# Optimization experiments

Hardware: AMD Instinct MI355X
Metric: run time of the kernel (lower is better)

Reference implementation:

```python
import jax, jax.numpy as jnp
import numpy as np

M = 4  # mixture size of the AttentionStem value embedding

def unfold_windows(a, kh, kw, Hout, Wout):
    # a: [..., Hp, Wp] -> [..., Hout, Wout, kh, kw] (stride-1 sliding windows, cropped)
    rows = []
    for i in range(kh):
        cols = [a[..., i:i + Hout, j:j + Wout] for j in range(kw)]
        rows.append(jnp.stack(cols, axis=-1))
    return jnp.stack(rows, axis=-2)

def attention_stem(x, qw, kw_, vw, emb_a, emb_b, emb_mix, kh, kw, pad):
    # x: [B,Cin,H,W]; qw/kw_: [Cin,Co]; vw: [M,Cin,Co]; emb_a:[Co,kh]; emb_b:[Co,kw]; emb_mix:[M,Co]
    B, Cin, H, W = x.shape
    pl, pr, pt, pb = pad  # F.pad order (left,right,top,bottom)
    xp = jnp.pad(x, ((0, 0), (0, 0), (pt, pb), (pl, pr)))
    Hp, Wp = xp.shape[2], xp.shape[3]
    Hout = min(Hp - kh + 1, H)
    Wout = min(Wp - kw + 1, W)
    q = jnp.einsum('bchw,co->bohw', x[:, :, :Hout, :Wout], qw)       # 1x1 conv query
    k = jnp.einsum('bchw,co->bohw', xp, kw_)                          # 1x1 conv key on padded
    v = jnp.einsum('bchw,mco->mbohw', xp, vw)                         # m 1x1 conv values
    k_win = unfold_windows(k, kh, kw, Hout, Wout)                     # [B,Co,Ho,Wo,kh,kw]
    v_win = unfold_windows(v, kh, kw, Hout, Wout)                     # [M,B,Co,Ho,Wo,kh,kw]
    # mixture relative-position embedding, softmax over mixtures per (kh,kw) offset
    la = emb_mix @ emb_a                                              # [M,kh]
    lb = emb_mix @ emb_b                                              # [M,kw]
    emb = jax.nn.softmax(la[:, :, None] + lb[:, None, :], axis=0)     # [M,kh,kw]
    v_agg = jnp.einsum('mkl,mbohwkl->bohwkl', emb, v_win)             # [B,Co,Ho,Wo,kh,kw]
    K = kh * kw
    scores = jnp.einsum('bohw,bohwkl->bhwkl', q, k_win).reshape(B, Hout, Wout, K)
    attn = jax.nn.softmax(scores, axis=-1).reshape(B, Hout, Wout, kh, kw)
    out = jnp.einsum('bhwkl,bohwkl->bohw', attn, v_agg)               # [B,Co,Ho,Wo]
    return out

def bn_relu(x, g, b):
    # training-mode BatchNorm2d + ReLU
    mu = x.mean(axis=(0, 2, 3), keepdims=True)
    var = x.var(axis=(0, 2, 3), keepdims=True)
    y = (x - mu) * jax.lax.rsqrt(var + 1e-5) * g[None, :, None, None] + b[None, :, None, None]
    return jax.nn.relu(y)

def _params(key):
    ks = jax.random.split(key, 18)
    def w(k, shape):
        return jax.random.normal(k, shape, dtype=jnp.float32) * 0.1
    cfg = [(1, 64, 1, 5), (64, 128, 2, 5), (128, 16, 2, 5)]
    p = {}
    i = 0
    for s, (ci, co, kh, kw) in enumerate(cfg):
        p[f'p{s}_q'] = w(ks[i], (ci, co)); i += 1
        p[f'p{s}_k'] = w(ks[i], (ci, co)); i += 1
        p[f'p{s}_v'] = w(ks[i], (M, ci, co)); i += 1
        p[f'p{s}_ea'] = w(ks[i], (co, kh)); i += 1
        p[f'p{s}_eb'] = w(ks[i], (co, kw)); i += 1
        p[f'p{s}_em'] = w(ks[i], (M, co)); i += 1
        p[f'p{s}_g'] = jnp.ones((co,), jnp.float32)
        p[f'p{s}_b'] = jnp.zeros((co,), jnp.float32)
    return p

def setup_inputs() -> dict:
    key = jax.random.key(0)
    kx, kp = jax.random.split(key)
    inp = {'x': jax.random.normal(kx, (2, 1, 8, 3000), dtype=jnp.float32)}
    inp.update(_params(kp))
    return inp

def reference(x,
              p0_q, p0_k, p0_v, p0_ea, p0_eb, p0_em, p0_g, p0_b,
              p1_q, p1_k, p1_v, p1_ea, p1_eb, p1_em, p1_g, p1_b,
              p2_q, p2_k, p2_v, p2_ea, p2_eb, p2_em, p2_g, p2_b):
    h = attention_stem(x, p0_q, p0_k, p0_v, p0_ea, p0_eb, p0_em, 1, 5, (2, 2, 0, 0))
    h = bn_relu(h, p0_g, p0_b)[:, :, ::2, ::2]                        # MaxPool2d(1,2) == stride-2 subsample
    h = attention_stem(h, p1_q, p1_k, p1_v, p1_ea, p1_eb, p1_em, 2, 5, (2, 2, 1, 1))
    h = bn_relu(h, p1_g, p1_b)[:, :, ::2, ::2]
    h = attention_stem(h, p2_q, p2_k, p2_v, p2_ea, p2_eb, p2_em, 2, 5, (2, 2, 0, 0))
    h = bn_relu(h, p2_g, p2_b)
    B, C, H, W = h.shape
    nW = W // 56                                                       # AvgPool2d((1,56))
    return h[:, :, :, :nW * 56].reshape(B, C, H, nW, 56).mean(-1)
```

## Files before the change

kernel.cpp:

```cpp
#include <hip/hip_runtime.h>
#include <math.h>


#define TPB 256

__global__ void prep0_kernel(const float* __restrict__ ea,
                             const float* __restrict__ eb,
                             const float* __restrict__ em,
                             const float* __restrict__ qw,
                             const float* __restrict__ kw_,
                             const float* __restrict__ vw,
                             float* __restrict__ par) {
    const int M4 = 4, Co = 64, kw = 5;
    __shared__ float la[4];
    __shared__ float lb[20];
    __shared__ float embs[20];
    int tid = threadIdx.x;
    if (tid < 64) {
        float p = qw[tid] * kw_[tid];
#pragma unroll
        for (int d = 1; d < 64; d <<= 1) p += __shfl_xor(p, d, 64);
        if (tid == 0) par[0] = p;
    }
    if (tid >= 64 && tid < 64 + M4) {
        int m = tid - 64;
        float s = 0.f;
        for (int o = 0; o < Co; ++o) s += em[m * Co + o] * ea[o];
        la[m] = s;
    }
    if (tid >= 128 && tid < 128 + M4 * kw) {
        int r = tid - 128;
        int m = r / kw, l = r % kw;
        float s = 0.f;
        for (int o = 0; o < Co; ++o) s += em[m * Co + o] * eb[o * kw + l];
        lb[m * kw + l] = s;
    }
    __syncthreads();
    if (tid < 5) {
        float lg[4];
        float mx = -1e30f;
        for (int m = 0; m < M4; ++m) {
            lg[m] = la[m] + lb[m * kw + tid];
            mx = fmaxf(mx, lg[m]);
        }
        float sum = 0.f;
        for (int m = 0; m < M4; ++m) { lg[m] = expf(lg[m] - mx); sum += lg[m]; }
        float inv = 1.f / sum;
        for (int m = 0; m < M4; ++m) embs[tid * 4 + m] = lg[m] * inv;
    }
    __syncthreads();
    for (int e = tid; e < 5 * 64; e += blockDim.x) {
        int t = e / 64, o = e - t * 64;
        float s = 0.f;
        for (int m = 0; m < M4; ++m) s += embs[t * 4 + m] * vw[m * 64 + o];
        par[1 + e] = s;
    }
}

__global__ void prep_wcat_kernel(const float* __restrict__ ea,
                                 const float* __restrict__ eb,
                                 const float* __restrict__ em,
                                 const float* __restrict__ qw,
                                 const float* __restrict__ kw_,
                                 const float* __restrict__ vw,
                                 float* __restrict__ Wcat,
                                 int Co, int kh, int kw, int Cin,
                                 const float2* __restrict__ part,
                                 float* __restrict__ mr,
                                 int Cprev, int NCH, int count) {
    const int M4 = 4;
    __shared__ float la[8];
    __shared__ float lb[20];
    __shared__ float embs[40];
    int K = kh * kw;
    int tid = threadIdx.x;
    if (blockIdx.x == 0 && tid < Cprev) {
        double s = 0.0, s2 = 0.0;
        for (int i = 0; i < NCH; ++i) {
            float2 p = part[(size_t)tid * NCH + i];
            s += p.x; s2 += p.y;
        }
        double mean = s / count;
        double var = s2 / count - mean * mean;
        mr[tid] = (float)mean;
        mr[Cprev + tid] = (float)(1.0 / sqrt(var + 1e-5));
    }
    if (tid < M4 * kh) {
        int m = tid / kh, k = tid % kh;
        float s = 0.f;
        for (int o = 0; o < Co; ++o) s += em[m * Co + o] * ea[o * kh + k];
        la[tid] = s;
    }
    if (tid >= 64 && tid < 64 + M4 * kw) {
        int r = tid - 64;
        int m = r / kw, l = r % kw;
        float s = 0.f;
        for (int o = 0; o < Co; ++o) s += em[m * Co + o] * eb[o * kw + l];
        lb[r] = s;
    }
    __syncthreads();
    if (tid < K) {
        int k = tid / kw, l = tid % kw;
        float lg[4];
        float mx = -1e30f;
        for (int m = 0; m < M4; ++m) {
            lg[m] = la[m * kh + k] + lb[m * kw + l];
            mx = fmaxf(mx, lg[m]);
        }
        float sum = 0.f;
        for (int m = 0; m < M4; ++m) { lg[m] = expf(lg[m] - mx); sum += lg[m]; }
        float inv = 1.f / sum;
        for (int m = 0; m < M4; ++m) embs[tid * 4 + m] = lg[m] * inv;
    }
    __syncthreads();
    int Mtot = (2 + K) * Co;
    long long total = (long long)Mtot * Cin;
    for (long long e = (long long)blockIdx.x * blockDim.x + tid; e < total;
         e += (long long)gridDim.x * blockDim.x) {
        int m = (int)(e / Cin);
        int c = (int)(e - (long long)m * Cin);
        float val;
        if (m < Co) {
            val = qw[c * Co + m];
        } else if (m < 2 * Co) {
            val = kw_[c * Co + (m - Co)];
        } else {
            int mz = m - 2 * Co;
            int t = mz / Co;
            int o = mz - t * Co;
            val = 0.f;
            for (int mm = 0; mm < M4; ++mm)
                val += embs[t * 4 + mm] * vw[(mm * Cin + c) * Co + o];
        }
        Wcat[e] = val;
    }
}

__global__ void attn_out0_kernel(const float* __restrict__ x,
                                 const float* __restrict__ par,
                                 float* __restrict__ s0,
                                 float2* __restrict__ part0) {
    __shared__ float wsh[5][256];
    __shared__ float vsh[5 * 64];
    int tid = threadIdx.x;
    int b = blockIdx.y;
    int n0 = blockIdx.x * 256;
    int n = n0 + tid;
    for (int i = tid; i < 320; i += 256) vsh[i] = par[1 + i];
    float c0 = par[0];
    if (n < 24000) {
        int h = n / 3000, w = n - h * 3000;
        const float* xr = x + b * 24000 + h * 3000;
        float xc = xr[w];
        float xs[5], s[5];
#pragma unroll
        for (int t = 0; t < 5; ++t) {
            int col = w + t - 2;
            xs[t] = (col >= 0 && col < 3000) ? xr[col] : 0.f;
            s[t] = c0 * xc * xs[t];
        }
        float mx = s[0];
#pragma unroll
        for (int t = 1; t < 5; ++t) mx = fmaxf(mx, s[t]);
        float sum = 0.f;
#pragma unroll
        for (int t = 0; t < 5; ++t) { s[t] = expf(s[t] - mx); sum += s[t]; }
        float inv = 1.f / sum;
#pragma unroll
        for (int t = 0; t < 5; ++t) wsh[t][tid] = s[t] * inv * xs[t];
    } else {
#pragma unroll
        for (int t = 0; t < 5; ++t) wsh[t][tid] = 0.f;
    }
    __syncthreads();
    int jq = tid & 63, og = tid >> 6;
    int nq = n0 + jq * 4;
    bool st = (nq < 24000);
    float wq[5][4];
#pragma unroll
    for (int t = 0; t < 5; ++t)
#pragma unroll
        for (int j = 0; j < 4; ++j) wq[t][j] = wsh[t][jq * 4 + j];
    int obase = og * 16;
    int chunk = b * gridDim.x + blockIdx.x;
    for (int oi = 0; oi < 16; ++oi) {
        int o = obase + oi;
        float4 v = make_float4(0.f, 0.f, 0.f, 0.f);
#pragma unroll
        for (int t = 0; t < 5; ++t) {
            float vo = vsh[t * 64 + o];
            v.x = fmaf(wq[t][0], vo, v.x);
            v.y = fmaf(wq[t][1], vo, v.y);
            v.z = fmaf(wq[t][2], vo, v.z);
            v.w = fmaf(wq[t][3], vo, v.w);
        }
        if (st) *(float4*)&s0[((size_t)b * 64 + o) * 24000 + nq] = v;
        float ls = v.x + v.y + v.z + v.w;
        float ls2 = v.x * v.x + v.y * v.y + v.z * v.z + v.w * v.w;
#pragma unroll
        for (int d = 1; d < 64; d <<= 1) {
            ls += __shfl_xor(ls, d, 64);
            ls2 += __shfl_xor(ls2, d, 64);
        }
        if ((tid & 63) == 0)
            part0[(size_t)o * 188 + chunk] = make_float2(ls, ls2);
    }
}

__launch_bounds__(256, 4)
__global__ void gemm_qkz_kernel(const float* __restrict__ A,
                                const float* __restrict__ X,
                                float* __restrict__ qk,
                                float* __restrict__ z,
                                int M, int N, int K, int twoCo) {
    __shared__ float As[32][132];
    __shared__ float Bs[32][132];
    int tid = threadIdx.x;
    int b = blockIdx.z;
    int m0 = blockIdx.y * 128, n0 = blockIdx.x * 128;
    int Mz = M - twoCo;
    float acc[8][8] = {{0.f}};
    int am = tid >> 1, ak = (tid & 1) * 16;
    int bk = tid >> 3, bn = (tid & 7) * 16;
    int tm = tid & 15, tn = tid >> 4;

    for (int k0 = 0; k0 < K; k0 += 32) {
        {
            int mA = m0 + am;
            const float* Ap = A + (size_t)mA * K + k0 + ak;
#pragma unroll
            for (int q = 0; q < 4; ++q) {
                float4 v = (mA < M) ? *(const float4*)(Ap + q * 4)
                                    : make_float4(0.f, 0.f, 0.f, 0.f);
                int kk = ak + q * 4;
                As[kk + 0][am] = v.x;
                As[kk + 1][am] = v.y;
                As[kk + 2][am] = v.z;
                As[kk + 3][am] = v.w;
            }
        }
        {
            const float* Xp = X + (size_t)b * K * N + (size_t)(k0 + bk) * N + n0 + bn;
            if (n0 + 128 <= N) {
#pragma unroll
                for (int q = 0; q < 4; ++q)
                    *(float4*)&Bs[bk][bn + q * 4] = *(const float4*)(Xp + q * 4);
            } else {
#pragma unroll
                for (int q = 0; q < 16; ++q) {
                    int n = n0 + bn + q;
                    Bs[bk][bn + q] = (n < N) ? Xp[q] : 0.f;
                }
            }
        }
        __syncthreads();
#pragma unroll 8
        for (int k = 0; k < 32; ++k) {
            float4 a0 = *(const float4*)&As[k][tm * 4];
            float4 a1 = *(const float4*)&As[k][64 + tm * 4];
            float4 b0 = *(const float4*)&Bs[k][tn * 4];
            float4 b1 = *(const float4*)&Bs[k][64 + tn * 4];
            float av[8] = {a0.x, a0.y, a0.z, a0.w, a1.x, a1.y, a1.z, a1.w};
            float bv[8] = {b0.x, b0.y, b0.z, b0.w, b1.x, b1.y, b1.z, b1.w};
#pragma unroll
            for (int i = 0; i < 8; ++i)
#pragma unroll
                for (int j = 0; j < 8; ++j)
                    acc[i][j] = fmaf(av[i], bv[j], acc[i][j]);
        }
        __syncthreads();
    }
    bool fullN = (n0 + 128 <= N);
#pragma unroll
    for (int iq = 0; iq < 2; ++iq) {
        int mb = m0 + iq * 64 + tm * 4;
        if (mb >= M) continue;
        if (mb < twoCo) {
#pragma unroll
            for (int jq = 0; jq < 2; ++jq)
#pragma unroll
                for (int jj = 0; jj < 4; ++jj) {
                    int n = n0 + jq * 64 + tn * 4 + jj;
                    if (n < N) {
                        float4 v = make_float4(acc[iq * 4 + 0][jq * 4 + jj],
                                               acc[iq * 4 + 1][jq * 4 + jj],
                                               acc[iq * 4 + 2][jq * 4 + jj],
                                               acc[iq * 4 + 3][jq * 4 + jj]);
                        *(float4*)&qk[((size_t)b * N + n) * twoCo + mb] = v;
                    }
                }
        } else {
#pragma unroll
            for (int i = 0; i < 4; ++i) {
                int row = mb + i - twoCo;
                float* zp = &z[((size_t)b * Mz + row) * N];
#pragma unroll
                for (int jq = 0; jq < 2; ++jq) {
                    int nb_ = n0 + jq * 64 + tn * 4;
                    if (fullN) {
                        *(float4*)&zp[nb_] = make_float4(acc[iq * 4 + i][jq * 4 + 0],
                                                         acc[iq * 4 + i][jq * 4 + 1],
                                                         acc[iq * 4 + i][jq * 4 + 2],
                                                         acc[iq * 4 + i][jq * 4 + 3]);
                    } else {
#pragma unroll
                        for (int jj = 0; jj < 4; ++jj)
                            if (nb_ + jj < N) zp[nb_ + jj] = acc[iq * 4 + i][jq * 4 + jj];
                    }
                }
            }
        }
    }
}

template <int KH, int KW, int CO, int NPB>
__global__ void attn_v3_kernel(const float* __restrict__ qk,
                               float* __restrict__ attn,
                               int H, int W, int Ho, int Wo, int pt, int pl) {
    const int K = KH * KW;
    __shared__ float ssh[NPB][K];
    int tid = threadIdx.x;
    int b = blockIdx.y;
    int ln = tid / K, t = tid - ln * K;
    int Nout = Ho * Wo;
    int n = blockIdx.x * NPB + ln;
    bool active = (tid < NPB * K) && (n < Nout);
    int HWin = H * W;
    float sv = 0.f;
    if (active) {
        int ho = n / Wo, wo = n - ho * Wo;
        int row = ho + t / KW - pt, col = wo + t % KW - pl;
        if (row >= 0 && row < H && col >= 0 && col < W) {
            const float* qp = qk + ((size_t)b * HWin + ho * W + wo) * (2 * CO);
            const float* kp = qk + ((size_t)b * HWin + (size_t)row * W + col) * (2 * CO) + CO;
#pragma unroll
            for (int o = 0; o < CO; o += 4) {
                float4 q4 = *(const float4*)(qp + o);
                float4 k4 = *(const float4*)(kp + o);
                sv += q4.x * k4.x + q4.y * k4.y + q4.z * k4.z + q4.w * k4.w;
            }
        }
        ssh[ln][t] = sv;
    }
    __syncthreads();
    if (active) {
        float mx = ssh[ln][0];
#pragma unroll
        for (int tt = 1; tt < K; ++tt) mx = fmaxf(mx, ssh[ln][tt]);
        float sum = 0.f;
#pragma unroll
        for (int tt = 0; tt < K; ++tt) sum += expf(ssh[ln][tt] - mx);
        float num = expf(sv - mx);
        attn[((size_t)b * K + t) * Nout + n] = num / sum;
    }
}

template <int KH, int KW>
__global__ void combine_stats_kernel(const float* __restrict__ z,
                                     const float* __restrict__ attn,
                                     float* __restrict__ out,
                                     float2* __restrict__ part,
                                     int Co, int Mz,
                                     int H, int W, int Ho, int Wo,
                                     int pt, int pl) {
    const int K = KH * KW;
    int tid = threadIdx.x;
    int bc = blockIdx.y;
    int b = bc / Co, o = bc - b * Co;
    int Nout = Ho * Wo, Nin = H * W;
    int n = blockIdx.x * blockDim.x + tid;
    float val = 0.f;
    if (n < Nout) {
        int ho = n / Wo, wo = n - ho * Wo;
#pragma unroll
        for (int dk = 0; dk < KH; ++dk) {
            int row = ho + dk - pt;
            if (row < 0 || row >= H) continue;
#pragma unroll
            for (int dl = 0; dl < KW; ++dl) {
                int col = wo + dl - pl;
                if (col < 0 || col >= W) continue;
                int t = dk * KW + dl;
                float a = attn[((size_t)b * K + t) * Nout + n];
                float zv = z[((size_t)b * Mz + t * Co + o) * Nin + row * W + col];
                val = fmaf(a, zv, val);
            }
        }
        out[((size_t)b * Co + o) * Nout + n] = val;
    }
    __shared__ float sh[TPB], sh2[TPB];
    sh[tid] = (n < Nout) ? val : 0.f;
    sh2[tid] = (n < Nout) ? val * val : 0.f;
    __syncthreads();
    for (int st = TPB / 2; st > 0; st >>= 1) {
        if (tid < st) { sh[tid] += sh[tid + st]; sh2[tid] += sh2[tid + st]; }
        __syncthreads();
    }
    if (tid == 0) {
        int chunk = b * gridDim.x + blockIdx.x;
        part[(size_t)o * (2 * gridDim.x) + chunk] = make_float2(sh[0], sh2[0]);
    }
}

__global__ void bn_pool_kernel(const float* __restrict__ x,
                               const float* __restrict__ mr,
                               const float* __restrict__ g,
                               const float* __restrict__ bb,
                               float* __restrict__ y,
                               int B, int C, int H, int W, int H2, int W2) {
    int idx = blockIdx.x * blockDim.x + threadIdx.x;
    int N = B * C * H2 * W2;
    if (idx >= N) return;
    int w2 = idx % W2; int r = idx / W2;
    int h2 = r % H2; r /= H2;
    int c = r % C; int b = r / C;
    float v = x[(((long long)b * C + c) * H + 2 * h2) * W + 2 * w2];
    float yn = (v - mr[c]) * mr[C + c] * g[c] + bb[c];
    y[idx] = fmaxf(yn, 0.f);
}

__global__ void bn_avg_final_kernel(const float* __restrict__ x,
                                    const float2* __restrict__ part,
                                    const float* __restrict__ g,
                                    const float* __restrict__ bb,
                                    float* __restrict__ out,
                                    int B, int C, int W, int nW, int NCH) {
    int idx = blockIdx.x * blockDim.x + threadIdx.x;
    int N = B * C * nW;
    if (idx >= N) return;
    int j = idx % nW; int r = idx / nW;
    int c = r % C; int b = r / C;
    double s = 0.0, s2 = 0.0;
    for (int i = 0; i < NCH; ++i) {
        float2 p = part[(size_t)c * NCH + i];
        s += p.x; s2 += p.y;
    }
    double cnt = (double)B * W;
    double mean = s / cnt;
    double var = s2 / cnt - mean * mean;
    float rstd = (float)(1.0 / sqrt(var + 1e-5));
    float meanf = (float)mean, gg = g[c], bo = bb[c];
    const float* xb = x + ((long long)b * C + c) * W + j * 56;
    float acc = 0.f;
    for (int i = 0; i < 56; ++i) {
        float yn = (xb[i] - meanf) * rstd * gg + bo;
        acc += fmaxf(yn, 0.f);
    }
    out[idx] = acc * (1.f / 56.f);
}

extern "C" void kernel_launch(void* const* d_in, const int* in_sizes, int n_in,
                              void* d_out, int out_size, void* d_ws, size_t ws_size,
                              hipStream_t stream) {
    const float* x   = (const float*)d_in[0];
    const float* qw0 = (const float*)d_in[1];
    const float* kw0 = (const float*)d_in[2];
    const float* vw0 = (const float*)d_in[3];
    const float* ea0 = (const float*)d_in[4];
    const float* eb0 = (const float*)d_in[5];
    const float* em0 = (const float*)d_in[6];
    const float* g0  = (const float*)d_in[7];
    const float* b0  = (const float*)d_in[8];
    const float* qw1 = (const float*)d_in[9];
    const float* kw1 = (const float*)d_in[10];
    const float* vw1 = (const float*)d_in[11];
    const float* ea1 = (const float*)d_in[12];
    const float* eb1 = (const float*)d_in[13];
    const float* em1 = (const float*)d_in[14];
    const float* g1  = (const float*)d_in[15];
    const float* b1  = (const float*)d_in[16];
    const float* qw2 = (const float*)d_in[17];
    const float* kw2 = (const float*)d_in[18];
    const float* vw2 = (const float*)d_in[19];
    const float* ea2 = (const float*)d_in[20];
    const float* eb2 = (const float*)d_in[21];
    const float* em2 = (const float*)d_in[22];
    const float* g2  = (const float*)d_in[23];
    const float* b2  = (const float*)d_in[24];
    float* outp = (float*)d_out;
    (void)ws_size; (void)in_sizes; (void)n_in; (void)out_size;

    float* ws = (float*)d_ws;
    size_t off = 0;
    auto alloc = [&](size_t n) { float* p = ws + off; off += (n + 63) & ~(size_t)63; return p; };

    float* arena = alloc(2 * 1280 * 6000);
    float* s0    = arena;
    float* z1    = arena;

    float* par0   = alloc(321);
    float* part0  = alloc(64 * 188 * 2);
    float* part1  = alloc(128 * 48 * 2);
    float* part2  = alloc(16 * 6 * 2);
    float* mr0    = alloc(2 * 64);
    float* h0     = alloc(2 * 64 * 6000);
    float* Wcat1  = alloc(1536 * 64);
    float* qk1    = alloc(2 * 6000 * 256);
    float* attn1  = alloc(2 * 10 * 6000);
    float* s1     = alloc(2 * 128 * 6000);
    float* mr1    = alloc(2 * 128);
    float* h1     = alloc(2 * 128 * 1500);
    float* Wcat2  = alloc(192 * 128);
    float* qk2    = alloc(2 * 1500 * 32);
    float* z2     = alloc(2 * 160 * 1500);
    float* attn2  = alloc(2 * 10 * 750);
    float* s2     = alloc(2 * 16 * 750);

    auto grid = [](int n) { return (n + TPB - 1) / TPB; };

    prep0_kernel<<<1, TPB, 0, stream>>>(ea0, eb0, em0, qw0, kw0, vw0, par0);
    {
        dim3 g(94, 2);
        attn_out0_kernel<<<g, TPB, 0, stream>>>(x, par0, s0, (float2*)part0);
    }
    prep_wcat_kernel<<<96, TPB, 0, stream>>>(ea1, eb1, em1, qw1, kw1, vw1, Wcat1,
        128, 2, 5, 64, (const float2*)part0, mr0, 64, 188, 48000);
    bn_pool_kernel<<<grid(2 * 64 * 6000), TPB, 0, stream>>>(s0, mr0, g0, b0, h0,
        2, 64, 8, 3000, 4, 1500);

    {
        dim3 g((6000 + 127) / 128, 1536 / 128, 2);
        gemm_qkz_kernel<<<g, TPB, 0, stream>>>(Wcat1, h0, qk1, z1, 1536, 6000, 64, 256);
    }
    {
        dim3 g(6000 / 25, 2);
        attn_v3_kernel<2, 5, 128, 25><<<g, TPB, 0, stream>>>(qk1, attn1,
            4, 1500, 4, 1500, 1, 2);
    }
    {
        dim3 g(24, 2 * 128);
        combine_stats_kernel<2, 5><<<g, TPB, 0, stream>>>(z1, attn1, s1,
            (float2*)part1, 128, 1280, 4, 1500, 4, 1500, 1, 2);
    }
    prep_wcat_kernel<<<24, TPB, 0, stream>>>(ea2, eb2, em2, qw2, kw2, vw2, Wcat2,
        16, 2, 5, 128, (const float2*)part1, mr1, 128, 48, 12000);
    bn_pool_kernel<<<grid(2 * 128 * 1500), TPB, 0, stream>>>(s1, mr1, g1, b1, h1,
        2, 128, 4, 1500, 2, 750);

    {
        dim3 g((1500 + 127) / 128, (192 + 127) / 128, 2);
        gemm_qkz_kernel<<<g, TPB, 0, stream>>>(Wcat2, h1, qk2, z2, 192, 1500, 128, 32);
    }
    {
        dim3 g(750 / 25, 2);
        attn_v3_kernel<2, 5, 16, 25><<<g, TPB, 0, stream>>>(qk2, attn2,
            2, 750, 1, 750, 0, 2);
    }
    {
        dim3 g(3, 2 * 16);
        combine_stats_kernel<2, 5><<<g, TPB, 0, stream>>>(z2, attn2, s2,
            (float2*)part2, 16, 160, 2, 750, 1, 750, 0, 2);
    }
    bn_avg_final_kernel<<<grid(2 * 16 * 13), TPB, 0, stream>>>(s2, (const float2*)part2,
        g2, b2, outp, 2, 16, 750, 13, 6);
}
```

Baseline: 282.2 us.

## Fuse BN+ReLU into GEMMs and replace stage-1 value path with attention-weighted GEMM

Stage 0 now writes only the stride-2 subsampled raw output instead of the full activation. BatchNorm+ReLU is applied on the fly inside the q/k GEMM and a new value GEMM, which drops the separate bn_pool passes. The value GEMM folds the attention weights into its B operand, so the large z1 tensor (1280 channels) is never materialised. It also writes only the subsampled output and emits per-block BN statistics. The cost is irregular gathers in the vgemm B-tile loads and small 64x64 tiles.

```diff
diff --git a/kernel.cpp b/kernel.cpp
--- a/kernel.cpp
+++ b/kernel.cpp
@@ -54,6 +54,154 @@
         float s = 0.f;
         for (int m = 0; m < M4; ++m) s += embs[t * 4 + m] * vw[m * 64 + o];
         par[1 + e] = s;
+    }
+}
+
+__global__ void attn_out0_kernel(const float* __restrict__ x,
+                                 const float* __restrict__ par,
+                                 float* __restrict__ h0raw,
+                                 float2* __restrict__ part0) {
+    __shared__ float wsh[5][256];
+    __shared__ float vsh[5 * 64];
+    int tid = threadIdx.x;
+    int b = blockIdx.y;
+    int n0 = blockIdx.x * 256;
+    int n = n0 + tid;
+    for (int i = tid; i < 320; i += 256) vsh[i] = par[1 + i];
+    float c0 = par[0];
+    if (n < 24000) {
+        int h = n / 3000, w = n - h * 3000;
+        const float* xr = x + b * 24000 + h * 3000;
+        float xc = xr[w];
+        float xs[5], s[5];
+#pragma unroll
+        for (int t = 0; t < 5; ++t) {
+            int col = w + t - 2;
+            xs[t] = (col >= 0 && col < 3000) ? xr[col] : 0.f;
+            s[t] = c0 * xc * xs[t];
+        }
+        float mx = s[0];
+#pragma unroll
+        for (int t = 1; t < 5; ++t) mx = fmaxf(mx, s[t]);
+        float sum = 0.f;
+#pragma unroll
+        for (int t = 0; t < 5; ++t) { s[t] = expf(s[t] - mx); sum += s[t]; }
+        float inv = 1.f / sum;
+#pragma unroll
+        for (int t = 0; t < 5; ++t) wsh[t][tid] = s[t] * inv * xs[t];
+    } else {
+#pragma unroll
+        for (int t = 0; t < 5; ++t) wsh[t][tid] = 0.f;
+    }
+    __syncthreads();
+    int jq = tid & 63, og = tid >> 6;
+    int nq = n0 + jq * 4;
+    int h = nq / 3000, w0 = nq - h * 3000;
+    bool st = (nq < 24000) && ((h & 1) == 0);
+    float wq[5][4];
+#pragma unroll
+    for (int t = 0; t < 5; ++t)
+#pragma unroll
+        for (int j = 0; j < 4; ++j) wq[t][j] = wsh[t][jq * 4 + j];
+    int obase = og * 16;
+    int chunk = b * gridDim.x + blockIdx.x;
+    for (int oi = 0; oi < 16; ++oi) {
+        int o = obase + oi;
+        float4 v = make_float4(0.f, 0.f, 0.f, 0.f);
+#pragma unroll
+        for (int t = 0; t < 5; ++t) {
+            float vo = vsh[t * 64 + o];
+            v.x = fmaf(wq[t][0], vo, v.x);
+            v.y = fmaf(wq[t][1], vo, v.y);
+            v.z = fmaf(wq[t][2], vo, v.z);
+            v.w = fmaf(wq[t][3], vo, v.w);
+        }
+        if (st) {
+            size_t base = ((size_t)b * 64 + o) * 6000 + (h >> 1) * 1500 + (w0 >> 1);
+            *(float2*)&h0raw[base] = make_float2(v.x, v.z);
+        }
+        float ls = v.x + v.y + v.z + v.w;
+        float ls2 = v.x * v.x + v.y * v.y + v.z * v.z + v.w * v.w;
+#pragma unroll
+        for (int d = 1; d < 64; d <<= 1) {
+            ls += __shfl_xor(ls, d, 64);
+            ls2 += __shfl_xor(ls2, d, 64);
+        }
+        if ((tid & 63) == 0)
+            part0[(size_t)o * 188 + chunk] = make_float2(ls, ls2);
+    }
+}
+
+__global__ void prep_stage1_kernel(const float* __restrict__ ea,
+                                   const float* __restrict__ eb,
+                                   const float* __restrict__ em,
+                                   const float* __restrict__ qw,
+                                   const float* __restrict__ kw_,
+                                   const float* __restrict__ vw,
+                                   float* __restrict__ Wqk,
+                                   float* __restrict__ Av,
+                                   const float2* __restrict__ part0,
+                                   float* __restrict__ mr0) {
+    const int M4 = 4, Co = 128, kh = 2, kw = 5, Cin = 64;
+    __shared__ float la[8];
+    __shared__ float lb[20];
+    __shared__ float embs[40];
+    int tid = threadIdx.x;
+    if (blockIdx.x == 0 && tid < 64) {
+        double s = 0.0, s2 = 0.0;
+        for (int i = 0; i < 188; ++i) {
+            float2 p = part0[(size_t)tid * 188 + i];
+            s += p.x; s2 += p.y;
+        }
+        double mean = s / 48000.0;
+        double var = s2 / 48000.0 - mean * mean;
+        mr0[tid] = (float)mean;
+        mr0[64 + tid] = (float)(1.0 / sqrt(var + 1e-5));
+    }
+    if (tid < M4 * kh) {
+        int m = tid / kh, k = tid % kh;
+        float s = 0.f;
+        for (int o = 0; o < Co; ++o) s += em[m * Co + o] * ea[o * kh + k];
+        la[tid] = s;
+    }
+    if (tid >= 64 && tid < 64 + M4 * kw) {
+        int r = tid - 64;
+        int m = r / kw, l = r % kw;
+        float s = 0.f;
+        for (int o = 0; o < Co; ++o) s += em[m * Co + o] * eb[o * kw + l];
+        lb[r] = s;
+    }
+    __syncthreads();
+    if (tid < 10) {
+        int k = tid / kw, l = tid % kw;
+        float lg[4];
+        float mx = -1e30f;
+        for (int m = 0; m < M4; ++m) {
+            lg[m] = la[m * kh + k] + lb[m * kw + l];
+            mx = fmaxf(mx, lg[m]);
+        }
+        float sum = 0.f;
+        for (int m = 0; m < M4; ++m) { lg[m] = expf(lg[m] - mx); sum += lg[m]; }
+        float inv = 1.f / sum;
+        for (int m = 0; m < M4; ++m) embs[tid * 4 + m] = lg[m] * inv;
+    }
+    __syncthreads();
+    const int TOT1 = 256 * 64;
+    const int TOT2 = 640 * 128;
+    for (int e = blockIdx.x * blockDim.x + tid; e < TOT1 + TOT2;
+         e += gridDim.x * blockDim.x) {
+        if (e < TOT1) {
+            int m = e / Cin, c = e - m * Cin;
+            Wqk[e] = (m < Co) ? qw[c * Co + m] : kw_[c * Co + (m - Co)];
+        } else {
+            int e2 = e - TOT1;
+            int k = e2 / Co, o = e2 - k * Co;
+            int c = k / 10, t = k - c * 10;
+            float val = 0.f;
+            for (int m = 0; m < M4; ++m)
+                val += embs[t * 4 + m] * vw[(m * Cin + c) * Co + o];
+            Av[e2] = val;
+        }
     }
 }
 
@@ -136,85 +284,18 @@
     }
 }
 
-__global__ void attn_out0_kernel(const float* __restrict__ x,
-                                 const float* __restrict__ par,
-                                 float* __restrict__ s0,
-                                 float2* __restrict__ part0) {
-    __shared__ float wsh[5][256];
-    __shared__ float vsh[5 * 64];
-    int tid = threadIdx.x;
-    int b = blockIdx.y;
-    int n0 = blockIdx.x * 256;
-    int n = n0 + tid;
-    for (int i = tid; i < 320; i += 256) vsh[i] = par[1 + i];
-    float c0 = par[0];
-    if (n < 24000) {
-        int h = n / 3000, w = n - h * 3000;
-        const float* xr = x + b * 24000 + h * 3000;
-        float xc = xr[w];
-        float xs[5], s[5];
-#pragma unroll
-        for (int t = 0; t < 5; ++t) {
-            int col = w + t - 2;
-            xs[t] = (col >= 0 && col < 3000) ? xr[col] : 0.f;
-            s[t] = c0 * xc * xs[t];
-        }
-        float mx = s[0];
-#pragma unroll
-        for (int t = 1; t < 5; ++t) mx = fmaxf(mx, s[t]);
-        float sum = 0.f;
-#pragma unroll
-        for (int t = 0; t < 5; ++t) { s[t] = expf(s[t] - mx); sum += s[t]; }
-        float inv = 1.f / sum;
-#pragma unroll
-        for (int t = 0; t < 5; ++t) wsh[t][tid] = s[t] * inv * xs[t];
-    } else {
-#pragma unroll
-        for (int t = 0; t < 5; ++t) wsh[t][tid] = 0.f;
-    }
-    __syncthreads();
-    int jq = tid & 63, og = tid >> 6;
-    int nq = n0 + jq * 4;
-    bool st = (nq < 24000);
-    float wq[5][4];
-#pragma unroll
-    for (int t = 0; t < 5; ++t)
-#pragma unroll
-        for (int j = 0; j < 4; ++j) wq[t][j] = wsh[t][jq * 4 + j];
-    int obase = og * 16;
-    int chunk = b * gridDim.x + blockIdx.x;
-    for (int oi = 0; oi < 16; ++oi) {
-        int o = obase + oi;
-        float4 v = make_float4(0.f, 0.f, 0.f, 0.f);
-#pragma unroll
-        for (int t = 0; t < 5; ++t) {
-            float vo = vsh[t * 64 + o];
-            v.x = fmaf(wq[t][0], vo, v.x);
-            v.y = fmaf(wq[t][1], vo, v.y);
-            v.z = fmaf(wq[t][2], vo, v.z);
-            v.w = fmaf(wq[t][3], vo, v.w);
-        }
-        if (st) *(float4*)&s0[((size_t)b * 64 + o) * 24000 + nq] = v;
-        float ls = v.x + v.y + v.z + v.w;
-        float ls2 = v.x * v.x + v.y * v.y + v.z * v.z + v.w * v.w;
-#pragma unroll
-        for (int d = 1; d < 64; d <<= 1) {
-            ls += __shfl_xor(ls, d, 64);
-            ls2 += __shfl_xor(ls2, d, 64);
-        }
-        if ((tid & 63) == 0)
-            part0[(size_t)o * 188 + chunk] = make_float2(ls, ls2);
-    }
-}
-
 __launch_bounds__(256, 4)
-__global__ void gemm_qkz_kernel(const float* __restrict__ A,
-                                const float* __restrict__ X,
-                                float* __restrict__ qk,
-                                float* __restrict__ z,
-                                int M, int N, int K, int twoCo) {
+__global__ void gemm_qkbn_kernel(const float* __restrict__ A,
+                                 const float* __restrict__ xraw,
+                                 const float* __restrict__ mr,
+                                 const float* __restrict__ g,
+                                 const float* __restrict__ bb,
+                                 float* __restrict__ qk,
+                                 float* __restrict__ z,
+                                 int M, int N, int K, int twoCo) {
     __shared__ float As[32][132];
     __shared__ float Bs[32][132];
+    __shared__ float scale[128], shift[128];
     int tid = threadIdx.x;
     int b = blockIdx.z;
     int m0 = blockIdx.y * 128, n0 = blockIdx.x * 128;
@@ -223,6 +304,12 @@
     int am = tid >> 1, ak = (tid & 1) * 16;
     int bk = tid >> 3, bn = (tid & 7) * 16;
     int tm = tid & 15, tn = tid >> 4;
+    for (int c = tid; c < K; c += 256) {
+        float sc = mr[K + c] * g[c];
+        scale[c] = sc;
+        shift[c] = bb[c] - mr[c] * sc;
+    }
+    __syncthreads();
 
     for (int k0 = 0; k0 < K; k0 += 32) {
         {
@@ -240,16 +327,24 @@
             }
         }
         {
-            const float* Xp = X + (size_t)b * K * N + (size_t)(k0 + bk) * N + n0 + bn;
+            int c = k0 + bk;
+            float sc = scale[c], sf = shift[c];
+            const float* Xp = xraw + ((size_t)b * K + c) * N + n0 + bn;
             if (n0 + 128 <= N) {
 #pragma unroll
-                for (int q = 0; q < 4; ++q)
-                    *(float4*)&Bs[bk][bn + q * 4] = *(const float4*)(Xp + q * 4);
+                for (int q = 0; q < 4; ++q) {
+                    float4 v = *(const float4*)(Xp + q * 4);
+                    v.x = fmaxf(fmaf(v.x, sc, sf), 0.f);
+                    v.y = fmaxf(fmaf(v.y, sc, sf), 0.f);
+                    v.z = fmaxf(fmaf(v.z, sc, sf), 0.f);
+                    v.w = fmaxf(fmaf(v.w, sc, sf), 0.f);
+                    *(float4*)&Bs[bk][bn + q * 4] = v;
+                }
             } else {
 #pragma unroll
                 for (int q = 0; q < 16; ++q) {
                     int n = n0 + bn + q;
-                    Bs[bk][bn + q] = (n < N) ? Xp[q] : 0.f;
+                    Bs[bk][bn + q] = (n < N) ? fmaxf(fmaf(Xp[q], sc, sf), 0.f) : 0.f;
                 }
             }
         }
@@ -356,6 +451,119 @@
 }
 
 template <int KH, int KW>
+__launch_bounds__(256)
+__global__ void vgemm_kernel(const float* __restrict__ Av,
+                             const float* __restrict__ xraw,
+                             const float* __restrict__ attn,
+                             const float* __restrict__ mr,
+                             const float* __restrict__ g,
+                             const float* __restrict__ bb,
+                             float* __restrict__ outsub,
+                             float2* __restrict__ part,
+                             int Cin, int Co,
+                             int H, int W, int Ho, int Wo,
+                             int pt, int pl, int Wsub) {
+    const int KK = KH * KW;
+    const int BK = 4 * KK;
+    __shared__ float As[BK][68];
+    __shared__ float Bs[BK][68];
+    __shared__ float scale[128], shift[128];
+    __shared__ float attn_s[KK][64];
+    __shared__ int ho_s[64], wo_s[64];
+    __shared__ float2 red[64][17];
+    int tid = threadIdx.x;
+    int b = blockIdx.z;
+    int m0 = blockIdx.y * 64;
+    int n0 = blockIdx.x * 64;
+    int Nin = H * W, Nout = Ho * Wo;
+    for (int c = tid; c < Cin; c += 256) {
+        float sc = mr[Cin + c] * g[c];
+        scale[c] = sc;
+        shift[c] = bb[c] - mr[c] * sc;
+    }
+    for (int e = tid; e < KK * 64; e += 256) {
+        int t = e >> 6, j = e & 63;
+        int n = n0 + j;
+        attn_s[t][j] = (n < Nout) ? attn[((size_t)b * KK + t) * Nout + n] : 0.f;
+    }
+    if (tid < 64) {
+        int n = n0 + tid;
+        ho_s[tid] = n / Wo;
+        wo_s[tid] = n % Wo;
+    }
+    __syncthreads();
+    float acc[4][4] = {{0.f}};
+    int tm = tid & 15, tn = tid >> 4;
+    int Ktot = Cin * KK;
+    for (int k0 = 0; k0 < Ktot; k0 += BK) {
+        int c0 = k0 / KK;
+#pragma unroll
+        for (int it = 0; it < 10; ++it) {
+            int e = it * 256 + tid;
+            int kk = e >> 6, mm = e & 63;
+            As[kk][mm] = Av[(size_t)(k0 + kk) * Co + m0 + mm];
+        }
+#pragma unroll
+        for (int it = 0; it < 10; ++it) {
+            int e = it * 256 + tid;
+            int kk = e >> 6, j = e & 63;
+            int cc = c0 + kk / KK, t = kk % KK;
+            int dk = t / KW, dl = t % KW;
+            int row = ho_s[j] + dk - pt;
+            int col = wo_s[j] + dl - pl;
+            float v = 0.f;
+            if ((n0 + j) < Nout && row >= 0 && row < H && col >= 0 && col < W) {
+                float xv = xraw[((size_t)b * Cin + cc) * Nin + row * W + col];
+                xv = fmaxf(fmaf(xv, scale[cc], shift[cc]), 0.f);
+                v = xv * attn_s[t][j];
+            }
+            Bs[kk][j] = v;
+        }
+        __syncthreads();
+#pragma unroll 8
+        for (int k = 0; k < BK; ++k) {
+            float4 a4 = *(const float4*)&As[k][tm * 4];
+            float4 b4 = *(const float4*)&Bs[k][tn * 4];
+            float av[4] = {a4.x, a4.y, a4.z, a4.w};
+            float bv[4] = {b4.x, b4.y, b4.z, b4.w};
+#pragma unroll
+            for (int i = 0; i < 4; ++i)
+#pragma unroll
+                for (int j = 0; j < 4; ++j)
+                    acc[i][j] = fmaf(av[i], bv[j], acc[i][j]);
+        }
+        __syncthreads();
+    }
+    int Nsub = ((Ho + 1) / 2) * Wsub;
+#pragma unroll
+    for (int i = 0; i < 4; ++i) {
+        int o = m0 + tm * 4 + i;
+        float s = 0.f, s2 = 0.f;
+#pragma unroll
+        for (int j = 0; j < 4; ++j) {
+            float v = acc[i][j];
+            s += v; s2 += v * v;
+            int jj = tn * 4 + j;
+            int n = n0 + jj;
+            if (n < Nout) {
+                int ho = ho_s[jj], wo = wo_s[jj];
+                if (((ho | wo) & 1) == 0)
+                    outsub[((size_t)b * Co + o) * Nsub + (ho >> 1) * Wsub + (wo >> 1)] = v;
+            }
+        }
+        red[tm * 4 + i][tn] = make_float2(s, s2);
+    }
+    __syncthreads();
+    if (tid < 64) {
+        float s = 0.f, s2 = 0.f;
+#pragma unroll
+        for (int q = 0; q < 16; ++q) { float2 p = red[tid][q]; s += p.x; s2 += p.y; }
+        int NCH = gridDim.x * gridDim.z;
+        part[(size_t)(m0 + tid) * NCH + b * gridDim.x + blockIdx.x] = make_float2(s, s2);
+    }
+}
+
+template <int KH, int KW>
 __global__ void combine_stats_kernel(const float* __restrict__ z,
                                      const float* __restrict__ attn,
                                      float* __restrict__ out,
@@ -400,23 +608,6 @@
         int chunk = b * gridDim.x + blockIdx.x;
         part[(size_t)o * (2 * gridDim.x) + chunk] = make_float2(sh[0], sh2[0]);
     }
-}
-
-__global__ void bn_pool_kernel(const float* __restrict__ x,
-                               const float* __restrict__ mr,
-                               const float* __restrict__ g,
-                               const float* __restrict__ bb,
-                               float* __restrict__ y,
-                               int B, int C, int H, int W, int H2, int W2) {
-    int idx = blockIdx.x * blockDim.x + threadIdx.x;
-    int N = B * C * H2 * W2;
-    if (idx >= N) return;
-    int w2 = idx % W2; int r = idx / W2;
-    int h2 = r % H2; r /= H2;
-    int c = r % C; int b = r / C;
-    float v = x[(((long long)b * C + c) * H + 2 * h2) * W + 2 * w2];
-    float yn = (v - mr[c]) * mr[C + c] * g[c] + bb[c];
-    y[idx] = fmaxf(yn, 0.f);
 }
 
 __global__ void bn_avg_final_kernel(const float* __restrict__ x,
@@ -484,26 +675,22 @@
     size_t off = 0;
     auto alloc = [&](size_t n) { float* p = ws + off; off += (n + 63) & ~(size_t)63; return p; };
 
-    float* arena = alloc(2 * 1280 * 6000);
-    float* s0    = arena;
-    float* z1    = arena;
-
     float* par0   = alloc(321);
     float* part0  = alloc(64 * 188 * 2);
-    float* part1  = alloc(128 * 48 * 2);
-    float* part2  = alloc(16 * 6 * 2);
-    float* mr0    = alloc(2 * 64);
-    float* h0     = alloc(2 * 64 * 6000);
-    float* Wcat1  = alloc(1536 * 64);
+    float* mr0    = alloc(128);
+    float* h0raw  = alloc(2 * 64 * 6000);
+    float* Wqk1   = alloc(256 * 64);
+    float* Av1    = alloc(640 * 128);
     float* qk1    = alloc(2 * 6000 * 256);
     float* attn1  = alloc(2 * 10 * 6000);
-    float* s1     = alloc(2 * 128 * 6000);
-    float* mr1    = alloc(2 * 128);
-    float* h1     = alloc(2 * 128 * 1500);
+    float* part1  = alloc(128 * 188 * 2);
+    float* mr1    = alloc(256);
+    float* h1raw  = alloc(2 * 128 * 1500);
     float* Wcat2  = alloc(192 * 128);
     float* qk2    = alloc(2 * 1500 * 32);
     float* z2     = alloc(2 * 160 * 1500);
     float* attn2  = alloc(2 * 10 * 750);
+    float* part2  = alloc(16 * 6 * 2);
     float* s2     = alloc(2 * 16 * 750);
 
     auto grid = [](int n) { return (n + TPB - 1) / TPB; };
@@ -511,16 +698,14 @@
     prep0_kernel<<<1, TPB, 0, stream>>>(ea0, eb0, em0, qw0, kw0, vw0, par0);
     {
         dim3 g(94, 2);
-        attn_out0_kernel<<<g, TPB, 0, stream>>>(x, par0, s0, (float2*)part0);
-    }
-    prep_wcat_kernel<<<96, TPB, 0, stream>>>(ea1, eb1, em1, qw1, kw1, vw1, Wcat1,
-        128, 2, 5, 64, (const float2*)part0, mr0, 64, 188, 48000);
-    bn_pool_kernel<<<grid(2 * 64 * 6000), TPB, 0, stream>>>(s0, mr0, g0, b0, h0,
-        2, 64, 8, 3000, 4, 1500);
-
+        attn_out0_kernel<<<g, TPB, 0, stream>>>(x, par0, h0raw, (float2*)part0);
+    }
+    prep_stage1_kernel<<<64, TPB, 0, stream>>>(ea1, eb1, em1, qw1, kw1, vw1,
+        Wqk1, Av1, (const float2*)part0, mr0);
     {
-        dim3 g((6000 + 127) / 128, 1536 / 128, 2);
-        gemm_qkz_kernel<<<g, TPB, 0, stream>>>(Wcat1, h0, qk1, z1, 1536, 6000, 64, 256);
+        dim3 g(47, 2, 2);
+        gemm_qkbn_kernel<<<g, TPB, 0, stream>>>(Wqk1, h0raw, mr0, g0, b0,
+            qk1, qk1 , 256, 6000, 64, 256);
     }
     {
         dim3 g(6000 / 25, 2);
@@ -528,18 +713,16 @@
             4, 1500, 4, 1500, 1, 2);
     }
     {
-        dim3 g(24, 2 * 128);
-        combine_stats_kernel<2, 5><<<g, TPB, 0, stream>>>(z1, attn1, s1,
-            (float2*)part1, 128, 1280, 4, 1500, 4, 1500, 1, 2);
+        dim3 g(94, 2, 2);
+        vgemm_kernel<2, 5><<<g, TPB, 0, stream>>>(Av1, h0raw, attn1, mr0, g0, b0,
+            h1raw, (float2*)part1, 64, 128, 4, 1500, 4, 1500, 1, 2, 750);
     }
     prep_wcat_kernel<<<24, TPB, 0, stream>>>(ea2, eb2, em2, qw2, kw2, vw2, Wcat2,
-        16, 2, 5, 128, (const float2*)part1, mr1, 128, 48, 12000);
-    bn_pool_kernel<<<grid(2 * 128 * 1500), TPB, 0, stream>>>(s1, mr1, g1, b1, h1,
-        2, 128, 4, 1500, 2, 750);
-
+        16, 2, 5, 128, (const float2*)part1, mr1, 128, 188, 12000);
     {
-        dim3 g((1500 + 127) / 128, (192 + 127) / 128, 2);
-        gemm_qkz_kernel<<<g, TPB, 0, stream>>>(Wcat2, h1, qk2, z2, 192, 1500, 128, 32);
+        dim3 g(12, 2, 2);
+        gemm_qkbn_kernel<<<g, TPB, 0, stream>>>(Wcat2, h1raw, mr1, g1, b1,
+            qk2, z2, 192, 1500, 128, 32);
     }
     {
         dim3 g(750 / 25, 2);
```

Measured after the change: 336.5 us. +19.2%, slower.
